# Performance work log

Measured on AMD Instinct MI355X. Metric: run time of the kernel, lower is better.

Reference implementation:

```python
import jax, jax.numpy as jnp
import numpy as np

B, T = 32, 64            # batch, max_timesteps
D_EMB, D_CONTENT, D_STYLE = 512, 128, 16
VOCAB = 32000
TEMP = 1.0
SOS_IDX = 0


def setup_inputs() -> dict:
    key = jax.random.key(0)
    ks = jax.random.split(key, 8)
    s = 0.02  # small init scale to keep softmax well-conditioned
    d_in = D_EMB + D_CONTENT + D_STYLE
    return {
        "content": jax.random.normal(ks[0], (B, D_CONTENT), jnp.float32),
        "style": jax.random.normal(ks[1], (B, D_STYLE), jnp.float32),
        "E": jax.random.normal(ks[2], (VOCAB, D_EMB), jnp.float32) * s,
        "Wk": jax.random.normal(ks[3], (d_in, 4 * D_EMB), jnp.float32) * s,
        "Wr": jax.random.normal(ks[4], (D_EMB, 4 * D_EMB), jnp.float32) * s,
        "b": jnp.zeros((4 * D_EMB,), jnp.float32),
        "Ws": jax.random.normal(ks[5], (D_EMB, VOCAB), jnp.float32) * s,
        "bs": jnp.zeros((VOCAB,), jnp.float32),
    }


def reference(content, style, E, Wk, Wr, b, Ws, bs):
    sos_emb = jnp.broadcast_to(E[SOS_IDX], (B, D_EMB))  # start token embedding

    def step(carry, _):
        h, c, emb = carry
        x = jnp.concatenate([emb, content, style], axis=-1)   # [B, d_in]
        z = x @ Wk + h @ Wr + b                               # [B, 4*units]
        i, f, g, o = jnp.split(z, 4, axis=-1)                  # keras gate order i,f,c,o
        i = jax.nn.sigmoid(i)
        f = jax.nn.sigmoid(f)
        g = jnp.tanh(g)
        o = jax.nn.sigmoid(o)
        c = f * c + i * g
        h = o * jnp.tanh(c)
        logits = h @ Ws + bs                                   # [B, vocab]
        p = jax.nn.softmax(logits / TEMP, axis=-1)
        emb_next = p @ E                                       # soft embedding [B, d_emb]
        return (h, c, emb_next), emb_next

    h0 = jnp.zeros((B, D_EMB), content.dtype)
    c0 = jnp.zeros((B, D_EMB), content.dtype)
    _, embs = jax.lax.scan(step, (h0, c0, sos_emb), None, length=T - 1)
    # [T-1, B, D] -> [B, T-1, D]; prepend SOS embedding
    out = jnp.concatenate([sos_emb[:, None, :], jnp.transpose(embs, (1, 0, 2))], axis=1)
    return out  # [B, T, d_emb]
```

## Files before the change

kernel.cpp:

```cpp
#include <hip/hip_runtime.h>

#define T_STEPS 63
#define NWG 256
#define WG_SIZE 256
#define NA 32
#define NV 224
#define NJC 14
#define NDC 16
#define NHM 15

typedef float floatx4 __attribute__((ext_vector_type(4)));
typedef __bf16 bf16x8 __attribute__((ext_vector_type(8)));

__device__ __forceinline__ unsigned short f2bf(float x) {
  unsigned int u = __builtin_bit_cast(unsigned int, x);
  u += 0x7fffu + ((u >> 16) & 1u);
  return (unsigned short)(u >> 16);
}
__device__ __forceinline__ float sigmoidf(float x) {
  return 1.0f / (1.0f + __expf(-x));
}
__device__ __forceinline__ floatx4 mfma_bf16(bf16x8 a, bf16x8 b, floatx4 c) {
  return __builtin_amdgcn_mfma_f32_16x16x32_bf16(a, b, c, 0, 0, 0);
}
__device__ __forceinline__ floatx4 mfma_fp8(long a, long b, floatx4 c) {
  return __builtin_amdgcn_mfma_f32_16x16x32_fp8_fp8(a, b, c, 0, 0, 0);
}
__device__ __forceinline__ unsigned char f2fp8(float x) {
  return (unsigned char)(__builtin_amdgcn_cvt_pk_fp8_f32(x, x, 0, false) & 0xff);
}

__device__ __forceinline__ unsigned long long ald64(const void* p) {
  return __hip_atomic_load((const unsigned long long*)p, __ATOMIC_RELAXED, __HIP_MEMORY_SCOPE_AGENT);
}
__device__ __forceinline__ float aldf(const float* p) {
  return __hip_atomic_load(p, __ATOMIC_RELAXED, __HIP_MEMORY_SCOPE_AGENT);
}
__device__ __forceinline__ void astf(float* p, float v) {
  __hip_atomic_store(p, v, __ATOMIC_RELAXED, __HIP_MEMORY_SCOPE_AGENT);
}
__device__ __forceinline__ void astu16(unsigned short* p, unsigned short v) {
  __hip_atomic_store(p, v, __ATOMIC_RELAXED, __HIP_MEMORY_SCOPE_AGENT);
}
__device__ __forceinline__ void astu32(unsigned int* p, unsigned int v) {
  __hip_atomic_store(p, v, __ATOMIC_RELAXED, __HIP_MEMORY_SCOPE_AGENT);
}
__device__ __forceinline__ void astu8(unsigned char* p, unsigned char v) {
  __hip_atomic_store(p, v, __ATOMIC_RELAXED, __HIP_MEMORY_SCOPE_AGENT);
}
__device__ __forceinline__ void afaddf(float* p, float v) {
  __hip_atomic_fetch_add(p, v, __ATOMIC_RELAXED, __HIP_MEMORY_SCOPE_AGENT);
}
__device__ __forceinline__ void afaddi(int* p, int v) {
  __hip_atomic_fetch_add(p, v, __ATOMIC_RELAXED, __HIP_MEMORY_SCOPE_AGENT);
}
__device__ __forceinline__ bf16x8 ld_bf8_at(const void* p) {
  union { unsigned long long q[2]; bf16x8 v; } u;
  u.q[0] = ald64(p);
  u.q[1] = ald64((const char*)p + 8);
  return u.v;
}

__device__ __forceinline__ void signal_flag(int* f) {
  __builtin_amdgcn_s_waitcnt(0);
  __syncthreads();
  if (threadIdx.x == 0)
    __hip_atomic_fetch_add(f, 1, __ATOMIC_RELAXED, __HIP_MEMORY_SCOPE_AGENT);
}
__device__ __forceinline__ void wait_flag(const int* f, int target) {
  if (threadIdx.x == 0) {
    while (__hip_atomic_load(f, __ATOMIC_RELAXED, __HIP_MEMORY_SCOPE_AGENT) < target)
      __builtin_amdgcn_s_sleep(2);
  }
  __syncthreads();
}

__global__ void k_transpose(const float* __restrict__ in, unsigned short* __restrict__ out,
                            int R, int C, int ostride, int ooff) {
  __shared__ unsigned short tile[64][65];
  const int r0 = blockIdx.x << 6, c0 = blockIdx.y << 6;
  const int t = threadIdx.x;
  const int tr4 = t >> 6, tc = t & 63;
#pragma unroll
  for (int p = 0; p < 16; ++p) {
    int i = (p << 2) + tr4;
    int r = r0 + i;
    unsigned short v = 0;
    if (r < R) v = f2bf(in[(size_t)r * C + (c0 + tc)]);
    tile[i][tc] = v;
  }
  __syncthreads();
#pragma unroll
  for (int p = 0; p < 16; ++p) {
    int j = (p << 2) + tr4;
    int r = r0 + tc;
    if (r < R) out[(size_t)(c0 + j) * ostride + ooff + r] = tile[tc][j];
  }
}

__global__ void k_transpose_fp8(const float* __restrict__ in, unsigned char* __restrict__ out,
                                int R, int C, long OS) {
  __shared__ unsigned char tile[64][68];
  const int r0 = blockIdx.x << 6, c0 = blockIdx.y << 6;
  const int t = threadIdx.x;
  const int tr4 = t >> 6, tc = t & 63;
#pragma unroll
  for (int p = 0; p < 16; ++p) {
    int i = (p << 2) + tr4;
    int r = r0 + i;
    float v = (r < R) ? in[(size_t)r * C + (c0 + tc)] : 0.f;
    tile[i][tc] = f2fp8(v);
  }
  __syncthreads();
#pragma unroll
  for (int p = 0; p < 16; ++p) {
    int j = (p << 2) + tr4;
    out[(size_t)(c0 + j) * OS + r0 + tc] = tile[tc][j];
  }
}

__global__ void k_init(const float* __restrict__ content, const float* __restrict__ style,
                       const float* __restrict__ E, unsigned short* cs_bf, float* out) {
  const int stride = gridDim.x * blockDim.x;
  const int idx = blockIdx.x * blockDim.x + threadIdx.x;
  for (int i = idx; i < 32 * 160; i += stride) {
    int b = i / 160, k = i - b * 160;
    float v = 0.f;
    if (k < 128)      v = content[b * 128 + k];
    else if (k < 144) v = style[b * 16 + (k - 128)];
    cs_bf[i] = f2bf(v);
  }
  for (int i = idx; i < 32 * 512; i += stride) {
    int b = i >> 9, d = i & 511;
    out[(size_t)b * (64 * 512) + d] = E[d];
  }
}

#define SMEM_BYTES 160768
#define OFF_E8TS_L 73728
#define OFF_ELDS_L 147456
#define OFF_ZBUF_L 152576

__global__ void __launch_bounds__(WG_SIZE, 1) k_main(
    const float* __restrict__ bvec,
    const float* __restrict__ bs,
    const unsigned char* __restrict__ Ws8_g,
    const unsigned char* __restrict__ E8T_g,
    const unsigned short* __restrict__ WkrT,
    const unsigned short* __restrict__ cs_bf,
    const float* __restrict__ E,
    unsigned short* h_bufg,
    unsigned char* h8,
    unsigned short* emb_bf,
    unsigned char* e8g,
    float* Upart,
    float* Zbuf,
    int* hflag, int* eflag, int* qflag, int* pvflag,
    float* out)
{
  const int wg = blockIdx.x;
  const int t  = threadIdx.x;
  const int wv = t >> 6;
  const int lane = t & 63;
  const int q = lane >> 4;
  const int m16 = lane & 15;

  __shared__ __align__(16) char smem[SMEM_BYTES];
  unsigned char* lds_ws   = (unsigned char*)smem;
  unsigned char* lds_e8ts = (unsigned char*)(smem + OFF_E8TS_L);
  unsigned char* lds_e    = (unsigned char*)(smem + OFF_ELDS_L);
  unsigned short* lds_wkr = (unsigned short*)smem;
  float* zbuf = (float*)(smem + OFF_ZBUF_L);

  if (wg < NA) {
    for (int idx = t; idx < 64 * 148; idx += WG_SIZE) {
      int row = idx / 148, grp = idx - row * 148;
      int g = row >> 4, c = row & 15;
      int n = g * 512 + (wg << 4) + c;
      ulong2 v = *(const ulong2*)(WkrT + (size_t)n * 1184 + grp * 8);
      *(ulong2*)((char*)lds_wkr + row * 2384 + grp * 16) = v;
    }
    const int dl = t & 15;
    const float bias0 = bvec[0 * 512 + (wg << 4) + dl];
    const float bias1 = bvec[1 * 512 + (wg << 4) + dl];
    const float bias2 = bvec[2 * 512 + (wg << 4) + dl];
    const float bias3 = bvec[3 * 512 + (wg << 4) + dl];
    float c2[2] = {0.f, 0.f};
    __syncthreads();

    const int mt = wv & 1, g0 = (wv >> 1) << 1;
    const int row = mt * 16 + m16;
    const unsigned short* b0row = lds_wkr + (g0 * 16 + m16) * 1192;
    const unsigned short* b1row = lds_wkr + ((g0 + 1) * 16 + m16) * 1192;
    const int d = (wg << 4) + dl;
    const int dc_a = wg >> 1;
    const int dl32 = ((wg & 1) << 4) + dl;

    floatx4 accG0 = {0.f, 0.f, 0.f, 0.f}, accG1 = {0.f, 0.f, 0.f, 0.f};

    for (int s = 0; s < T_STEPS; ++s) {
      const int pc = s & 1;
      if (s == 0) {
#pragma unroll
        for (int ks = 16; ks < 21; ++ks) {
          bf16x8 a = *(const bf16x8*)(cs_bf + row * 160 + (ks - 16) * 32 + q * 8);
          accG0 = mfma_bf16(a, *(const bf16x8*)(b0row + ks * 32 + q * 8), accG0);
          accG1 = mfma_bf16(a, *(const bf16x8*)(b1row + ks * 32 + q * 8), accG1);
        }
#pragma unroll 4
        for (int ks = 0; ks < 16; ++ks) {
          const float* ep = E + ks * 32 + q * 8;
          bf16x8 a;
#pragma unroll
          for (int i = 0; i < 8; ++i) a[i] = (__bf16)ep[i];
          accG0 = mfma_bf16(a, *(const bf16x8*)(b0row + ks * 32 + q * 8), accG0);
          accG1 = mfma_bf16(a, *(const bf16x8*)(b1row + ks * 32 + q * 8), accG1);
        }
      } else {
        wait_flag(eflag + (s - 1) * 16, NA);
        if (t < NJC) astf(Zbuf + ((s - 1) & 1) * (NJC * 32) + t * 32 + wg, 0.0f);
#pragma unroll 8
        for (int ks = 0; ks < 16; ++ks) {
          bf16x8 a = ld_bf8_at(emb_bf + row * 512 + ks * 32 + q * 8);
          accG0 = mfma_bf16(a, *(const bf16x8*)(b0row + ks * 32 + q * 8), accG0);
          accG1 = mfma_bf16(a, *(const bf16x8*)(b1row + ks * 32 + q * 8), accG1);
        }
      }
#pragma unroll
      for (int r = 0; r < 4; ++r) {
        zbuf[(g0 * 32 + mt * 16 + q * 4 + r) * 16 + m16] = accG0[r];
        zbuf[((g0 + 1) * 32 + mt * 16 + q * 4 + r) * 16 + m16] = accG1[r];
      }
      __syncthreads();
#pragma unroll
      for (int pp = 0; pp < 2; ++pp) {
        const int b = (pp * 256 + t) >> 4;
        float zi = zbuf[(0 * 32 + b) * 16 + dl] + bias0;
        float zf = zbuf[(1 * 32 + b) * 16 + dl] + bias1;
        float zg = zbuf[(2 * 32 + b) * 16 + dl] + bias2;
        float zo = zbuf[(3 * 32 + b) * 16 + dl] + bias3;
        float iv = sigmoidf(zi), fv = sigmoidf(zf);
        float gv = tanhf(zg),    ov = sigmoidf(zo);
        c2[pp] = fv * c2[pp] + iv * gv;
        float h = ov * tanhf(c2[pp]);
        astu16(h_bufg + b * 512 + d, f2bf(h));
        astu8(h8 + b * 512 + d, f2fp8(h));
      }
      __builtin_amdgcn_s_waitcnt(0);
      __syncthreads();
      if (t < NHM) afaddi(hflag + (s * NHM + t) * 16, 1);
      if (s + 1 < T_STEPS) {
        wait_flag(hflag + (s * NHM + (NHM - 1)) * 16, NA);
        accG0 = floatx4{0.f, 0.f, 0.f, 0.f};
        accG1 = floatx4{0.f, 0.f, 0.f, 0.f};
#pragma unroll 8
        for (int ks = 21; ks < 37; ++ks) {
          bf16x8 a = ld_bf8_at(h_bufg + row * 512 + (ks - 21) * 32 + q * 8);
          accG0 = mfma_bf16(a, *(const bf16x8*)(b0row + ks * 32 + q * 8), accG0);
          accG1 = mfma_bf16(a, *(const bf16x8*)(b1row + ks * 32 + q * 8), accG1);
        }
#pragma unroll
        for (int ks = 16; ks < 21; ++ks) {
          bf16x8 a = *(const bf16x8*)(cs_bf + row * 160 + (ks - 16) * 32 + q * 8);
          accG0 = mfma_bf16(a, *(const bf16x8*)(b0row + ks * 32 + q * 8), accG0);
          accG1 = mfma_bf16(a, *(const bf16x8*)(b1row + ks * 32 + q * 8), accG1);
        }
      }
      wait_flag(pvflag + (s * NDC + dc_a) * 16, NJC);
      float evs[2];
#pragma unroll
      for (int pp = 0; pp < 2; ++pp) {
        const int b = (pp * 256 + t) >> 4;
        float uv = 0.f, Zv = 0.f;
        const float* up = Upart + ((size_t)(dc_a * NJC) * 32 + b) * 32 + dl32;
#pragma unroll
        for (int g = 0; g < NJC; ++g) uv += aldf(up + g * 1024);
#pragma unroll
        for (int g = 0; g < NJC; ++g) Zv += aldf(Zbuf + pc * (NJC * 32) + g * 32 + b);
        float ev = uv / Zv;
        evs[pp] = ev;
        astu16(emb_bf + b * 512 + d, f2bf(ev));
      }
      signal_flag(eflag + s * 16);
#pragma unroll
      for (int pp = 0; pp < 2; ++pp) {
        const int b = (pp * 256 + t) >> 4;
        out[(size_t)b * (64 * 512) + (size_t)(s + 1) * 512 + d] = evs[pp];
      }
    }
  } else {
    const int wgv = wg - NA;
    const int jc = wgv >> 4;
    const int dc = wgv & 15;
    const long j0 = (long)wgv * 144;
    for (int idx = t; idx < 144 * 64; idx += WG_SIZE) {
      int row = idx >> 6, grp = idx & 63;
      long v = *(const long*)(Ws8_g + (j0 + row) * 512 + grp * 8);
      *(long*)(lds_ws + row * 512 + ((grp ^ (row & 7)) << 3)) = v;
    }
    for (int idx = t; idx < 32 * 288; idx += WG_SIZE) {
      int dd = idx / 288, g = idx - dd * 288;
      long v = *(const long*)(E8T_g + (size_t)(dc * 32 + dd) * 32768 + (size_t)jc * 2304 + (size_t)g * 8);
      int g2 = g + dd; if (g2 >= 288) g2 -= 288;
      *(long*)(lds_e8ts + dd * 2304 + (g2 << 3)) = v;
    }
    for (int idx = t; idx < (32 * 160) / 8; idx += WG_SIZE) ((long*)lds_e)[idx] = 0;
    __syncthreads();

    for (int s = 0; s < T_STEPS; ++s) {
      wait_flag(hflag + (s * NHM + jc) * 16, NA);
      const int pc = s & 1;
      long ah[2][16];
#pragma unroll
      for (int mtl = 0; mtl < 2; ++mtl)
#pragma unroll
        for (int ks = 0; ks < 16; ++ks)
          ah[mtl][ks] = (long)ald64(h8 + (mtl * 16 + m16) * 512 + ks * 32 + q * 8);
      for (int tile = wv; tile < 9; tile += 4) {
        const int jl = tile * 16 + m16;
        const unsigned char* wrow = lds_ws + jl * 512;
        const int sw = jl & 7;
        floatx4 acc[2] = {{0,0,0,0},{0,0,0,0}};
#pragma unroll
        for (int ks = 0; ks < 16; ++ks) {
          int g = ks * 4 + q;
          long bfrag = *(const long*)(wrow + ((g ^ sw) << 3));
          acc[0] = mfma_fp8(ah[0][ks], bfrag, acc[0]);
          acc[1] = mfma_fp8(ah[1][ks], bfrag, acc[1]);
        }
        const long jg = j0 + jl;
        const float bsv = bs[jg < 32000 ? jg : 31999];
        const bool valid = (jg < 32000);
#pragma unroll
        for (int mtl = 0; mtl < 2; ++mtl)
#pragma unroll
          for (int r = 0; r < 4; ++r) {
            float e = valid ? __expf(acc[mtl][r] + bsv) : 0.0f;
            lds_e[(mtl * 16 + q * 4 + r) * 160 + jl] = f2fp8(e);
          }
      }
      __syncthreads();
      for (int idx = t; idx < 32 * 36; idx += WG_SIZE) {
        int b = idx / 36, g = idx - b * 36;
        unsigned int v = *(const unsigned int*)(lds_e + b * 160 + g * 4);
        astu32((unsigned int*)(e8g + (size_t)b * 32768 + j0 + g * 4), v);
      }
      if (t >= 192 && t < 224) {
        const int b = t - 192;
        const unsigned int* rowp = (const unsigned int*)(lds_e + b * 160);
        float z = 0.f;
        for (int g = 0; g < 36; ++g) {
          int w4 = (int)rowp[g];
          z += __builtin_amdgcn_cvt_f32_fp8(w4, 0) + __builtin_amdgcn_cvt_f32_fp8(w4, 1)
             + __builtin_amdgcn_cvt_f32_fp8(w4, 2) + __builtin_amdgcn_cvt_f32_fp8(w4, 3);
        }
        afaddf(Zbuf + pc * (NJC * 32) + jc * 32 + b, z);
      }
      signal_flag(qflag + (s * NJC + jc) * 16);
      wait_flag(qflag + (s * NJC + jc) * 16, 16);
      {
        const int mtp = wv & 1, ntl = wv >> 1;
        const int dl_local = ntl * 16 + m16;
        const unsigned char* erow = lds_e8ts + dl_local * 2304;
        const unsigned char* arow = e8g + (size_t)(mtp * 16 + m16) * 32768 + (size_t)jc * 2304;
        floatx4 acc0 = {0,0,0,0}, acc1 = {0,0,0,0};
#pragma unroll 8
        for (int ks = 0; ks < 72; ks += 2) {
          long a0 = (long)ald64(arow + ks * 32 + q * 8);
          long a1 = (long)ald64(arow + (ks + 1) * 32 + q * 8);
          int g0 = ks * 4 + q + dl_local; if (g0 >= 288) g0 -= 288;
          int g1 = g0 + 4;                if (g1 >= 288) g1 -= 288;
          acc0 = mfma_fp8(a0, *(const long*)(erow + (g0 << 3)), acc0);
          acc1 = mfma_fp8(a1, *(const long*)(erow + (g1 << 3)), acc1);
        }
        floatx4 accs = acc0 + acc1;
#pragma unroll
        for (int r = 0; r < 4; ++r)
          astf(Upart + ((size_t)(dc * NJC + jc) * 32 + (mtp * 16 + q * 4 + r)) * 32 + dl_local, accs[r]);
      }
      signal_flag(pvflag + (s * NDC + dc) * 16);
    }
  }
}

extern "C" void kernel_launch(void* const* d_in, const int* in_sizes, int n_in,
                              void* d_out, int out_size, void* d_ws, size_t ws_size,
                              hipStream_t stream) {
  const float* content = (const float*)d_in[0];
  const float* style   = (const float*)d_in[1];
  const float* E       = (const float*)d_in[2];
  const float* Wk      = (const float*)d_in[3];
  const float* Wr      = (const float*)d_in[4];
  const float* bvec    = (const float*)d_in[5];
  const float* Ws      = (const float*)d_in[6];
  const float* bs      = (const float*)d_in[7];
  float* out = (float*)d_out;
  char* ws = (char*)d_ws;

  constexpr size_t SZ_WS8  = 32256ull * 512;
  constexpr size_t SZ_E8T  = 512ull * 32768;
  constexpr size_t SZ_WKRT = 2048ull * 1184 * 2;
  constexpr size_t SZ_CS   = 32ull * 160 * 2;
  constexpr size_t SZ_HB   = 32ull * 512 * 2;
  constexpr size_t SZ_H8   = 32ull * 512;
  constexpr size_t SZ_E8G  = 32ull * 32768;
  constexpr size_t SZ_UP   = 16ull * 14 * 32 * 32 * 4;
  constexpr size_t SZ_ZB   = 2ull * 14 * 32 * 4;
  constexpr size_t SZ_HF   = 64ull * 15 * 16 * 4;
  constexpr size_t SZ_EF   = 64ull * 16 * 4;
  constexpr size_t SZ_QF   = 63ull * 14 * 16 * 4;
  constexpr size_t SZ_PF   = 63ull * 16 * 16 * 4;
  constexpr size_t SZ_EMB  = 32ull * 512 * 2;
  constexpr size_t OFF_WS8  = 0;
  constexpr size_t OFF_E8T  = OFF_WS8 + SZ_WS8;
  constexpr size_t OFF_WKRT = OFF_E8T + SZ_E8T;
  constexpr size_t OFF_CS   = OFF_WKRT + SZ_WKRT;
  constexpr size_t OFF_HB   = OFF_CS + SZ_CS;
  constexpr size_t OFF_H8   = OFF_HB + SZ_HB;
  constexpr size_t OFF_E8G  = OFF_H8 + SZ_H8;
  constexpr size_t OFF_UP   = OFF_E8G + SZ_E8G;
  constexpr size_t OFF_ZB   = OFF_UP + SZ_UP;
  constexpr size_t OFF_HF   = OFF_ZB + SZ_ZB;
  constexpr size_t OFF_EF   = OFF_HF + SZ_HF;
  constexpr size_t OFF_QF   = OFF_EF + SZ_EF;
  constexpr size_t OFF_PF   = OFF_QF + SZ_QF;
  constexpr size_t OFF_EMB  = OFF_PF + SZ_PF;

  unsigned char*  Ws8_g = (unsigned char*)(ws + OFF_WS8);
  unsigned char*  E8T_g = (unsigned char*)(ws + OFF_E8T);
  unsigned short* WkrT  = (unsigned short*)(ws + OFF_WKRT);
  unsigned short* cs_bf = (unsigned short*)(ws + OFF_CS);
  unsigned short* h_bufg= (unsigned short*)(ws + OFF_HB);
  unsigned char*  h8    = (unsigned char*)(ws + OFF_H8);
  unsigned char*  e8g   = (unsigned char*)(ws + OFF_E8G);
  float* Upart          = (float*)(ws + OFF_UP);
  float* Zbuf           = (float*)(ws + OFF_ZB);
  int* hflag            = (int*)(ws + OFF_HF);
  int* eflag            = (int*)(ws + OFF_EF);
  int* qflag            = (int*)(ws + OFF_QF);
  int* pvflag           = (int*)(ws + OFF_PF);
  unsigned short* emb_bf= (unsigned short*)(ws + OFF_EMB);

  hipMemsetAsync(Ws8_g, 0, SZ_WS8, stream);
  hipMemsetAsync(E8T_g, 0, SZ_E8T, stream);
  hipMemsetAsync(WkrT, 0, SZ_WKRT, stream);
  hipMemsetAsync(ws + OFF_ZB, 0, SZ_ZB + SZ_HF + SZ_EF + SZ_QF + SZ_PF, stream);

  k_transpose_fp8<<<dim3(8, 500), 256, 0, stream>>>(Ws, Ws8_g, 512, 32000, 512);
  k_transpose_fp8<<<dim3(500, 8), 256, 0, stream>>>(E, E8T_g, 32000, 512, 32768);
  k_transpose<<<dim3(11, 32), 256, 0, stream>>>(Wk, WkrT, 656, 2048, 1184, 0);
  k_transpose<<<dim3(8, 32), 256, 0, stream>>>(Wr, WkrT, 512, 2048, 1184, 672);
  k_init<<<64, 256, 0, stream>>>(content, style, E, cs_bf, out);

  void* args[] = { (void*)&bvec, (void*)&bs, (void*)&Ws8_g, (void*)&E8T_g, (void*)&WkrT,
                   (void*)&cs_bf, (void*)&E, (void*)&h_bufg, (void*)&h8, (void*)&emb_bf,
                   (void*)&e8g, (void*)&Upart, (void*)&Zbuf,
                   (void*)&hflag, (void*)&eflag, (void*)&qflag, (void*)&pvflag,
                   (void*)&out };
  hipLaunchCooperativeKernel((void*)k_main, dim3(NWG), dim3(WG_SIZE), args, 0, stream);

  (void)in_sizes; (void)n_in; (void)out_size; (void)ws_size;
}
```

Baseline: 2.072 ms.

## Precompute E·Wk product to feed soft-prob gate input directly, bypassing embedding round-trip

Precomputes M = E @ Wk_emb (vocab x 2048 gates) in fp8 during setup. Each vocab workgroup then multiplies its unnormalized softmax chunk by M to produce partial gate pre-activations, so the LSTM workgroups no longer wait for the normalized soft embedding before computing the next step's gates. The emb_bf handoff and its flag are removed, and the output writes are deferred by one step. The change also double-buffers the e8 and Upart buffers and replaces the sleep-based spin with a busy spin. In exchange it adds a large setup GEMM, an extra 32x2048 gate GEMM over the vocab each step, and fp8 rounding error in the gate inputs.

```diff
diff --git a/kernel.cpp b/kernel.cpp
--- a/kernel.cpp
+++ b/kernel.cpp
@@ -61,6 +61,9 @@
   return u.v;
 }
 
+__device__ __forceinline__ void spin_until(const int* f, int target) {
+  while (__hip_atomic_load(f, __ATOMIC_RELAXED, __HIP_MEMORY_SCOPE_AGENT) < target) { }
+}
 __device__ __forceinline__ void signal_flag(int* f) {
   __builtin_amdgcn_s_waitcnt(0);
   __syncthreads();
@@ -68,10 +71,7 @@
     __hip_atomic_fetch_add(f, 1, __ATOMIC_RELAXED, __HIP_MEMORY_SCOPE_AGENT);
 }
 __device__ __forceinline__ void wait_flag(const int* f, int target) {
-  if (threadIdx.x == 0) {
-    while (__hip_atomic_load(f, __ATOMIC_RELAXED, __HIP_MEMORY_SCOPE_AGENT) < target)
-      __builtin_amdgcn_s_sleep(2);
-  }
+  if (threadIdx.x == 0) spin_until(f, target);
   __syncthreads();
 }
 
@@ -99,7 +99,7 @@
 }
 
 __global__ void k_transpose_fp8(const float* __restrict__ in, unsigned char* __restrict__ out,
-                                int R, int C, long OS) {
+                                int R, int C, long OS, float scale) {
   __shared__ unsigned char tile[64][68];
   const int r0 = blockIdx.x << 6, c0 = blockIdx.y << 6;
   const int t = threadIdx.x;
@@ -108,7 +108,7 @@
   for (int p = 0; p < 16; ++p) {
     int i = (p << 2) + tr4;
     int r = r0 + i;
-    float v = (r < R) ? in[(size_t)r * C + (c0 + tc)] : 0.f;
+    float v = (r < R) ? in[(size_t)r * C + (c0 + tc)] * scale : 0.f;
     tile[i][tc] = f2fp8(v);
   }
   __syncthreads();
@@ -117,6 +117,56 @@
     int j = (p << 2) + tr4;
     out[(size_t)(c0 + j) * OS + r0 + tc] = tile[tc][j];
   }
+}
+
+__global__ void k_cast_e8(const float* __restrict__ E, unsigned char* __restrict__ E8) {
+  const int stride = gridDim.x * blockDim.x;
+  const int total = 32256 * 512 / 4;
+  for (int i = blockIdx.x * blockDim.x + threadIdx.x; i < total; i += stride) {
+    int row = i >> 7;
+    unsigned int w = 0;
+    if (row < 32000) {
+      const float* p = E + (size_t)i * 4;
+      int lo = __builtin_amdgcn_cvt_pk_fp8_f32(p[0] * 16.f, p[1] * 16.f, 0, false);
+      w = (unsigned int)__builtin_amdgcn_cvt_pk_fp8_f32(p[2] * 16.f, p[3] * 16.f, lo, true);
+    }
+    *(unsigned int*)(E8 + (size_t)i * 4) = w;
+  }
+}
+
+__global__ void __launch_bounds__(256) k_gemm_m(const unsigned char* __restrict__ Wk8T,
+                                               const unsigned char* __restrict__ E8,
+                                               unsigned char* __restrict__ MT8) {
+  const int j0 = blockIdx.x << 7, g0 = blockIdx.y << 7;
+  const int t = threadIdx.x, wv = t >> 6, lane = t & 63;
+  const int q = lane >> 4, m16 = lane & 15;
+  const int gtb = wv << 1;
+  floatx4 acc[2][8];
+#pragma unroll
+  for (int a = 0; a < 2; ++a)
+#pragma unroll
+    for (int b = 0; b < 8; ++b) acc[a][b] = floatx4{0.f, 0.f, 0.f, 0.f};
+#pragma unroll 4
+  for (int ks = 0; ks < 16; ++ks) {
+    long a0 = *(const long*)(Wk8T + (size_t)(g0 + gtb * 16 + m16) * 512 + ks * 32 + q * 8);
+    long a1 = *(const long*)(Wk8T + (size_t)(g0 + gtb * 16 + 16 + m16) * 512 + ks * 32 + q * 8);
+#pragma unroll
+    for (int jt = 0; jt < 8; ++jt) {
+      long b = *(const long*)(E8 + (size_t)(j0 + jt * 16 + m16) * 512 + ks * 32 + q * 8);
+      acc[0][jt] = mfma_fp8(a0, b, acc[0][jt]);
+      acc[1][jt] = mfma_fp8(a1, b, acc[1][jt]);
+    }
+  }
+#pragma unroll
+  for (int gt2 = 0; gt2 < 2; ++gt2)
+#pragma unroll
+    for (int jt = 0; jt < 8; ++jt)
+#pragma unroll
+      for (int r = 0; r < 4; ++r) {
+        int g = g0 + (gtb + gt2) * 16 + (q << 2) + r;
+        int j = j0 + jt * 16 + m16;
+        MT8[(size_t)g * 32768 + j] = f2fp8(acc[gt2][jt][r] * 0.5f);
+      }
 }
 
 __global__ void k_init(const float* __restrict__ content, const float* __restrict__ style,
@@ -149,13 +199,14 @@
     const unsigned short* __restrict__ WkrT,
     const unsigned short* __restrict__ cs_bf,
     const float* __restrict__ E,
+    const unsigned char* __restrict__ MT8,
     unsigned short* h_bufg,
     unsigned char* h8,
-    unsigned short* emb_bf,
     unsigned char* e8g,
     float* Upart,
+    float* Zp,
     float* Zbuf,
-    int* hflag, int* eflag, int* qflag, int* pvflag,
+    int* hflag, int* qflag, int* zflag, int* gflag, int* pvflag,
     float* out)
 {
   const int wg = blockIdx.x;
@@ -188,18 +239,20 @@
     float c2[2] = {0.f, 0.f};
     __syncthreads();
 
-    const int mt = wv & 1, g0 = (wv >> 1) << 1;
+    const int mt = wv & 1, g0w = (wv >> 1) << 1;
     const int row = mt * 16 + m16;
-    const unsigned short* b0row = lds_wkr + (g0 * 16 + m16) * 1192;
-    const unsigned short* b1row = lds_wkr + ((g0 + 1) * 16 + m16) * 1192;
+    const unsigned short* b0row = lds_wkr + (g0w * 16 + m16) * 1192;
+    const unsigned short* b1row = lds_wkr + ((g0w + 1) * 16 + m16) * 1192;
     const int d = (wg << 4) + dl;
     const int dc_a = wg >> 1;
     const int dl32 = ((wg & 1) << 4) + dl;
+    const int gcbase = wg >> 3;
 
     floatx4 accG0 = {0.f, 0.f, 0.f, 0.f}, accG1 = {0.f, 0.f, 0.f, 0.f};
+    float inv[2] = {0.f, 0.f};
+    float zr[2][4];
 
     for (int s = 0; s < T_STEPS; ++s) {
-      const int pc = s & 1;
       if (s == 0) {
 #pragma unroll
         for (int ks = 16; ks < 21; ++ks) {
@@ -217,19 +270,34 @@
           accG1 = mfma_bf16(a, *(const bf16x8*)(b1row + ks * 32 + q * 8), accG1);
         }
       } else {
-        wait_flag(eflag + (s - 1) * 16, NA);
-        if (t < NJC) astf(Zbuf + ((s - 1) & 1) * (NJC * 32) + t * 32 + wg, 0.0f);
-#pragma unroll 8
-        for (int ks = 0; ks < 16; ++ks) {
-          bf16x8 a = ld_bf8_at(emb_bf + row * 512 + ks * 32 + q * 8);
-          accG0 = mfma_bf16(a, *(const bf16x8*)(b0row + ks * 32 + q * 8), accG0);
-          accG1 = mfma_bf16(a, *(const bf16x8*)(b1row + ks * 32 + q * 8), accG1);
+        if (t < 4) spin_until(zflag + (((s - 1) * NDC + (t * 4 + gcbase)) << 4), NJC);
+        else if (t == 4) spin_until(gflag + ((s - 1) << 4), NA);
+        __syncthreads();
+        const int pc1 = (s - 1) & 1;
+#pragma unroll
+        for (int pp = 0; pp < 2; ++pp) {
+          const int b = (pp * 256 + t) >> 4;
+          const float* zp = Zp + (size_t)b * 2048 + (wg << 4) + dl;
+          float z0 = 0.f, z1 = 0.f, z2 = 0.f, z3 = 0.f, Zv = 0.f;
+#pragma unroll
+          for (int jc = 0; jc < NJC; ++jc) {
+            const float* p = zp + jc * 65536;
+            z0 += aldf(p);
+            z1 += aldf(p + 512);
+            z2 += aldf(p + 1024);
+            z3 += aldf(p + 1536);
+            Zv += aldf(Zbuf + pc1 * (NJC * 32) + jc * 32 + b);
+          }
+          float iv = 1.0f / (128.0f * Zv);
+          inv[pp] = iv;
+          zr[pp][0] = z0 * iv; zr[pp][1] = z1 * iv;
+          zr[pp][2] = z2 * iv; zr[pp][3] = z3 * iv;
         }
       }
 #pragma unroll
       for (int r = 0; r < 4; ++r) {
-        zbuf[(g0 * 32 + mt * 16 + q * 4 + r) * 16 + m16] = accG0[r];
-        zbuf[((g0 + 1) * 32 + mt * 16 + q * 4 + r) * 16 + m16] = accG1[r];
+        zbuf[(g0w * 32 + mt * 16 + q * 4 + r) * 16 + m16] = accG0[r];
+        zbuf[((g0w + 1) * 32 + mt * 16 + q * 4 + r) * 16 + m16] = accG1[r];
       }
       __syncthreads();
 #pragma unroll
@@ -239,6 +307,7 @@
         float zf = zbuf[(1 * 32 + b) * 16 + dl] + bias1;
         float zg = zbuf[(2 * 32 + b) * 16 + dl] + bias2;
         float zo = zbuf[(3 * 32 + b) * 16 + dl] + bias3;
+        if (s > 0) { zi += zr[pp][0]; zf += zr[pp][1]; zg += zr[pp][2]; zo += zr[pp][3]; }
         float iv = sigmoidf(zi), fv = sigmoidf(zf);
         float gv = tanhf(zg),    ov = sigmoidf(zo);
         c2[pp] = fv * c2[pp] + iv * gv;
@@ -248,9 +317,9 @@
       }
       __builtin_amdgcn_s_waitcnt(0);
       __syncthreads();
-      if (t < NHM) afaddi(hflag + (s * NHM + t) * 16, 1);
+      if (t < NHM) afaddi(hflag + ((s * NHM + t) << 4), 1);
       if (s + 1 < T_STEPS) {
-        wait_flag(hflag + (s * NHM + (NHM - 1)) * 16, NA);
+        wait_flag(hflag + ((s * NHM + (NHM - 1)) << 4), NA);
         accG0 = floatx4{0.f, 0.f, 0.f, 0.f};
         accG1 = floatx4{0.f, 0.f, 0.f, 0.f};
 #pragma unroll 8
@@ -265,51 +334,61 @@
           accG0 = mfma_bf16(a, *(const bf16x8*)(b0row + ks * 32 + q * 8), accG0);
           accG1 = mfma_bf16(a, *(const bf16x8*)(b1row + ks * 32 + q * 8), accG1);
         }
-      }
-      wait_flag(pvflag + (s * NDC + dc_a) * 16, NJC);
-      float evs[2];
+        signal_flag(gflag + (s << 4));
+      }
+      if (s >= 1) {
+        wait_flag(pvflag + (((s - 1) * NDC + dc_a) << 4), NJC);
+        const int pc1 = (s - 1) & 1;
+#pragma unroll
+        for (int pp = 0; pp < 2; ++pp) {
+          const int b = (pp * 256 + t) >> 4;
+          float uv = 0.f;
+          const float* up = Upart + (size_t)pc1 * 229376 + ((size_t)(dc_a * NJC) * 32 + b) * 32 + dl32;
+#pragma unroll
+          for (int jc = 0; jc < NJC; ++jc) uv += aldf(up + jc * 1024);
+          out[(size_t)b * (64 * 512) + (size_t)s * 512 + d] = uv * inv[pp] * 128.0f;
+        }
+        if (t < NJC) astf(Zbuf + pc1 * (NJC * 32) + t * 32 + wg, 0.0f);
+      }
+    }
+    {
+      wait_flag(pvflag + (((T_STEPS - 1) * NDC + dc_a) << 4), NJC);
+      const int pc1 = (T_STEPS - 1) & 1;
 #pragma unroll
       for (int pp = 0; pp < 2; ++pp) {
         const int b = (pp * 256 + t) >> 4;
         float uv = 0.f, Zv = 0.f;
-        const float* up = Upart + ((size_t)(dc_a * NJC) * 32 + b) * 32 + dl32;
-#pragma unroll
-        for (int g = 0; g < NJC; ++g) uv += aldf(up + g * 1024);
-#pragma unroll
-        for (int g = 0; g < NJC; ++g) Zv += aldf(Zbuf + pc * (NJC * 32) + g * 32 + b);
-        float ev = uv / Zv;
-        evs[pp] = ev;
-        astu16(emb_bf + b * 512 + d, f2bf(ev));
-      }
-      signal_flag(eflag + s * 16);
-#pragma unroll
-      for (int pp = 0; pp < 2; ++pp) {
-        const int b = (pp * 256 + t) >> 4;
-        out[(size_t)b * (64 * 512) + (size_t)(s + 1) * 512 + d] = evs[pp];
+        const float* up = Upart + (size_t)pc1 * 229376 + ((size_t)(dc_a * NJC) * 32 + b) * 32 + dl32;
+#pragma unroll
+        for (int jc = 0; jc < NJC; ++jc) {
+          uv += aldf(up + jc * 1024);
+          Zv += aldf(Zbuf + pc1 * (NJC * 32) + jc * 32 + b);
+        }
+        out[(size_t)b * (64 * 512) + (size_t)T_STEPS * 512 + d] = uv / Zv;
       }
     }
   } else {
     const int wgv = wg - NA;
     const int jc = wgv >> 4;
-    const int dc = wgv & 15;
+    const int gc = wgv & 15;
     const long j0 = (long)wgv * 144;
     for (int idx = t; idx < 144 * 64; idx += WG_SIZE) {
-      int row = idx >> 6, grp = idx & 63;
-      long v = *(const long*)(Ws8_g + (j0 + row) * 512 + grp * 8);
-      *(long*)(lds_ws + row * 512 + ((grp ^ (row & 7)) << 3)) = v;
+      int r2 = idx >> 6, grp = idx & 63;
+      long v = *(const long*)(Ws8_g + (j0 + r2) * 512 + grp * 8);
+      *(long*)(lds_ws + r2 * 512 + ((grp ^ (r2 & 7)) << 3)) = v;
     }
     for (int idx = t; idx < 32 * 288; idx += WG_SIZE) {
       int dd = idx / 288, g = idx - dd * 288;
-      long v = *(const long*)(E8T_g + (size_t)(dc * 32 + dd) * 32768 + (size_t)jc * 2304 + (size_t)g * 8);
+      long v = *(const long*)(E8T_g + (size_t)(gc * 32 + dd) * 32768 + (size_t)jc * 2304 + (size_t)g * 8);
       int g2 = g + dd; if (g2 >= 288) g2 -= 288;
       *(long*)(lds_e8ts + dd * 2304 + (g2 << 3)) = v;
     }
-    for (int idx = t; idx < (32 * 160) / 8; idx += WG_SIZE) ((long*)lds_e)[idx] = 0;
     __syncthreads();
 
     for (int s = 0; s < T_STEPS; ++s) {
-      wait_flag(hflag + (s * NHM + jc) * 16, NA);
+      wait_flag(hflag + ((s * NHM + jc) << 4), NA);
       const int pc = s & 1;
+      unsigned char* e8p = e8g + (size_t)pc * 1048576;
       long ah[2][16];
 #pragma unroll
       for (int mtl = 0; mtl < 2; ++mtl)
@@ -343,8 +422,10 @@
       for (int idx = t; idx < 32 * 36; idx += WG_SIZE) {
         int b = idx / 36, g = idx - b * 36;
         unsigned int v = *(const unsigned int*)(lds_e + b * 160 + g * 4);
-        astu32((unsigned int*)(e8g + (size_t)b * 32768 + j0 + g * 4), v);
-      }
+        astu32((unsigned int*)(e8p + (size_t)b * 32768 + j0 + g * 4), v);
+      }
+      signal_flag(qflag + ((s * NJC + jc) << 4));
+      wait_flag(qflag + ((s * NJC + jc) << 4), 16);
       if (t >= 192 && t < 224) {
         const int b = t - 192;
         const unsigned int* rowp = (const unsigned int*)(lds_e + b * 160);
@@ -356,29 +437,52 @@
         }
         afaddf(Zbuf + pc * (NJC * 32) + jc * 32 + b, z);
       }
-      signal_flag(qflag + (s * NJC + jc) * 16);
-      wait_flag(qflag + (s * NJC + jc) * 16, 16);
+      if (s < T_STEPS - 1) {
+        const int mtp = wv & 1, ggb = (wv >> 1) << 2;
+        const unsigned char* ab = e8p + (size_t)(mtp * 16 + m16) * 32768 + (size_t)jc * 2304;
+        const unsigned char* mb = MT8 + (size_t)(gc * 128 + ggb * 16 + m16) * 32768 + (size_t)jc * 2304;
+        floatx4 za0 = {0,0,0,0}, za1 = {0,0,0,0}, za2 = {0,0,0,0}, za3 = {0,0,0,0};
+#pragma unroll 4
+        for (int ks = 0; ks < 72; ++ks) {
+          long a = (long)ald64(ab + ks * 32 + q * 8);
+          long b0 = *(const long*)(mb + 0ull * 524288 + ks * 32 + q * 8);
+          long b1 = *(const long*)(mb + 1ull * 524288 + ks * 32 + q * 8);
+          long b2 = *(const long*)(mb + 2ull * 524288 + ks * 32 + q * 8);
+          long b3 = *(const long*)(mb + 3ull * 524288 + ks * 32 + q * 8);
+          za0 = mfma_fp8(a, b0, za0); za1 = mfma_fp8(a, b1, za1);
+          za2 = mfma_fp8(a, b2, za2); za3 = mfma_fp8(a, b3, za3);
+        }
+        const int brow = mtp * 16 + (q << 2);
+#pragma unroll
+        for (int r = 0; r < 4; ++r) {
+          float* zp = Zp + (size_t)(jc * 32 + brow + r) * 2048 + gc * 128 + ggb * 16 + m16;
+          astf(zp +  0, za0[r]); astf(zp + 16, za1[r]);
+          astf(zp + 32, za2[r]); astf(zp + 48, za3[r]);
+        }
+        signal_flag(zflag + ((s * NDC + gc) << 4));
+      }
       {
         const int mtp = wv & 1, ntl = wv >> 1;
         const int dl_local = ntl * 16 + m16;
         const unsigned char* erow = lds_e8ts + dl_local * 2304;
-        const unsigned char* arow = e8g + (size_t)(mtp * 16 + m16) * 32768 + (size_t)jc * 2304;
+        const unsigned char* arow = e8p + (size_t)(mtp * 16 + m16) * 32768 + (size_t)jc * 2304;
         floatx4 acc0 = {0,0,0,0}, acc1 = {0,0,0,0};
 #pragma unroll 8
         for (int ks = 0; ks < 72; ks += 2) {
           long a0 = (long)ald64(arow + ks * 32 + q * 8);
           long a1 = (long)ald64(arow + (ks + 1) * 32 + q * 8);
-          int g0 = ks * 4 + q + dl_local; if (g0 >= 288) g0 -= 288;
-          int g1 = g0 + 4;                if (g1 >= 288) g1 -= 288;
-          acc0 = mfma_fp8(a0, *(const long*)(erow + (g0 << 3)), acc0);
-          acc1 = mfma_fp8(a1, *(const long*)(erow + (g1 << 3)), acc1);
+          int g0i = ks * 4 + q + dl_local; if (g0i >= 288) g0i -= 288;
+          int g1i = g0i + 4;               if (g1i >= 288) g1i -= 288;
+          acc0 = mfma_fp8(a0, *(const long*)(erow + (g0i << 3)), acc0);
+          acc1 = mfma_fp8(a1, *(const long*)(erow + (g1i << 3)), acc1);
         }
         floatx4 accs = acc0 + acc1;
 #pragma unroll
         for (int r = 0; r < 4; ++r)
-          astf(Upart + ((size_t)(dc * NJC + jc) * 32 + (mtp * 16 + q * 4 + r)) * 32 + dl_local, accs[r]);
-      }
-      signal_flag(pvflag + (s * NDC + dc) * 16);
+          astf(Upart + (size_t)pc * 229376 +
+               ((size_t)(gc * NJC + jc) * 32 + (mtp * 16 + (q << 2) + r)) * 32 + dl_local, accs[r]);
+      }
+      signal_flag(pvflag + ((s * NDC + gc) << 4));
     }
   }
 }
@@ -403,28 +507,34 @@
   constexpr size_t SZ_CS   = 32ull * 160 * 2;
   constexpr size_t SZ_HB   = 32ull * 512 * 2;
   constexpr size_t SZ_H8   = 32ull * 512;
-  constexpr size_t SZ_E8G  = 32ull * 32768;
-  constexpr size_t SZ_UP   = 16ull * 14 * 32 * 32 * 4;
-  constexpr size_t SZ_ZB   = 2ull * 14 * 32 * 4;
-  constexpr size_t SZ_HF   = 64ull * 15 * 16 * 4;
-  constexpr size_t SZ_EF   = 64ull * 16 * 4;
-  constexpr size_t SZ_QF   = 63ull * 14 * 16 * 4;
-  constexpr size_t SZ_PF   = 63ull * 16 * 16 * 4;
-  constexpr size_t SZ_EMB  = 32ull * 512 * 2;
+  constexpr size_t SZ_ZB   = 2ull * NJC * 32 * 4;
+  constexpr size_t SZ_HF   = 63ull * NHM * 16 * 4;
+  constexpr size_t SZ_QF   = 63ull * NJC * 16 * 4;
+  constexpr size_t SZ_ZF   = 63ull * NDC * 16 * 4;
+  constexpr size_t SZ_GF   = 63ull * 16 * 4;
+  constexpr size_t SZ_PF   = 63ull * NDC * 16 * 4;
+  constexpr size_t SZ_E8   = 32256ull * 512;
+  constexpr size_t SZ_WK8T = 2048ull * 512;
+  constexpr size_t SZ_MT8  = 2048ull * 32768;
+
   constexpr size_t OFF_WS8  = 0;
   constexpr size_t OFF_E8T  = OFF_WS8 + SZ_WS8;
   constexpr size_t OFF_WKRT = OFF_E8T + SZ_E8T;
   constexpr size_t OFF_CS   = OFF_WKRT + SZ_WKRT;
   constexpr size_t OFF_HB   = OFF_CS + SZ_CS;
   constexpr size_t OFF_H8   = OFF_HB + SZ_HB;
-  constexpr size_t OFF_E8G  = OFF_H8 + SZ_H8;
-  constexpr size_t OFF_UP   = OFF_E8G + SZ_E8G;
-  constexpr size_t OFF_ZB   = OFF_UP + SZ_UP;
-  constexpr size_t OFF_HF   = OFF_ZB + SZ_ZB;
-  constexpr size_t OFF_EF   = OFF_HF + SZ_HF;
-  constexpr size_t OFF_QF   = OFF_EF + SZ_EF;
-  constexpr size_t OFF_PF   = OFF_QF + SZ_QF;
-  constexpr size_t OFF_EMB  = OFF_PF + SZ_PF;
+  constexpr size_t OFF_ZB   = OFF_H8 + SZ_H8;
+  constexpr size_t OFF_HFL  = OFF_ZB + SZ_ZB;
+  constexpr size_t OFF_QFL  = OFF_HFL + SZ_HF;
+  constexpr size_t OFF_ZFL  = OFF_QFL + SZ_QF;
+  constexpr size_t OFF_GFL  = OFF_ZFL + SZ_ZF;
+  constexpr size_t OFF_PFL  = OFF_GFL + SZ_GF;
+  constexpr size_t OFF_E8   = OFF_PFL + SZ_PF;
+  constexpr size_t OFF_E8G  = OFF_E8;
+  constexpr size_t OFF_UP   = OFF_E8 + 2097152;
+  constexpr size_t OFF_ZP   = OFF_E8 + 3932160;
+  constexpr size_t OFF_WK8T = OFF_E8 + SZ_E8;
+  constexpr size_t OFF_MT8  = OFF_WK8T + SZ_WK8T;
 
   unsigned char*  Ws8_g = (unsigned char*)(ws + OFF_WS8);
   unsigned char*  E8T_g = (unsigned char*)(ws + OFF_E8T);
@@ -432,30 +542,37 @@
   unsigned short* cs_bf = (unsigned short*)(ws + OFF_CS);
   unsigned short* h_bufg= (unsigned short*)(ws + OFF_HB);
   unsigned char*  h8    = (unsigned char*)(ws + OFF_H8);
+  float* Zbuf           = (float*)(ws + OFF_ZB);
+  int* hflag            = (int*)(ws + OFF_HFL);
+  int* qflag            = (int*)(ws + OFF_QFL);
+  int* zflag            = (int*)(ws + OFF_ZFL);
+  int* gflag            = (int*)(ws + OFF_GFL);
+  int* pvflag           = (int*)(ws + OFF_PFL);
+  unsigned char*  E8    = (unsigned char*)(ws + OFF_E8);
   unsigned char*  e8g   = (unsigned char*)(ws + OFF_E8G);
   float* Upart          = (float*)(ws + OFF_UP);
-  float* Zbuf           = (float*)(ws + OFF_ZB);
-  int* hflag            = (int*)(ws + OFF_HF);
-  int* eflag            = (int*)(ws + OFF_EF);
-  int* qflag            = (int*)(ws + OFF_QF);
-  int* pvflag           = (int*)(ws + OFF_PF);
-  unsigned short* emb_bf= (unsigned short*)(ws + OFF_EMB);
+  float* Zp             = (float*)(ws + OFF_ZP);
+  unsigned char*  Wk8T  = (unsigned char*)(ws + OFF_WK8T);
+  unsigned char*  MT8   = (unsigned char*)(ws + OFF_MT8);
 
   hipMemsetAsync(Ws8_g, 0, SZ_WS8, stream);
   hipMemsetAsync(E8T_g, 0, SZ_E8T, stream);
   hipMemsetAsync(WkrT, 0, SZ_WKRT, stream);
-  hipMemsetAsync(ws + OFF_ZB, 0, SZ_ZB + SZ_HF + SZ_EF + SZ_QF + SZ_PF, stream);
-
-  k_transpose_fp8<<<dim3(8, 500), 256, 0, stream>>>(Ws, Ws8_g, 512, 32000, 512);
-  k_transpose_fp8<<<dim3(500, 8), 256, 0, stream>>>(E, E8T_g, 32000, 512, 32768);
+  hipMemsetAsync(ws + OFF_ZB, 0, SZ_ZB + SZ_HF + SZ_QF + SZ_ZF + SZ_GF + SZ_PF, stream);
+
+  k_transpose_fp8<<<dim3(8, 500), 256, 0, stream>>>(Ws, Ws8_g, 512, 32000, 512, 1.0f);
+  k_transpose_fp8<<<dim3(500, 8), 256, 0, stream>>>(E, E8T_g, 32000, 512, 32768, 1.0f);
+  k_transpose_fp8<<<dim3(8, 32), 256, 0, stream>>>(Wk, Wk8T, 512, 2048, 512, 16.0f);
+  k_cast_e8<<<2048, 256, 0, stream>>>(E, E8);
+  k_gemm_m<<<dim3(252, 16), 256, 0, stream>>>(Wk8T, E8, MT8);
   k_transpose<<<dim3(11, 32), 256, 0, stream>>>(Wk, WkrT, 656, 2048, 1184, 0);
   k_transpose<<<dim3(8, 32), 256, 0, stream>>>(Wr, WkrT, 512, 2048, 1184, 672);
   k_init<<<64, 256, 0, stream>>>(content, style, E, cs_bf, out);
 
   void* args[] = { (void*)&bvec, (void*)&bs, (void*)&Ws8_g, (void*)&E8T_g, (void*)&WkrT,
-                   (void*)&cs_bf, (void*)&E, (void*)&h_bufg, (void*)&h8, (void*)&emb_bf,
-                   (void*)&e8g, (void*)&Upart, (void*)&Zbuf,
-                   (void*)&hflag, (void*)&eflag, (void*)&qflag, (void*)&pvflag,
+                   (void*)&cs_bf, (void*)&E, (void*)&MT8, (void*)&h_bufg, (void*)&h8,
+                   (void*)&e8g, (void*)&Upart, (void*)&Zp, (void*)&Zbuf,
+                   (void*)&hflag, (void*)&qflag, (void*)&zflag, (void*)&gflag, (void*)&pvflag,
                    (void*)&out };
   hipLaunchCooperativeKernel((void*)k_main, dim3(NWG), dim3(WG_SIZE), args, 0, stream);
 
```

Result: slower. 4.289 ms (+107.0%).

## Replace atomic counter flags with per-workgroup step stamps and wave-wide polling

Applied to the files above, without the earlier changes.

Cross-workgroup synchronisation moves from shared fetch-add counters, polled by one thread with sleeps, to per-workgroup step stamps. Each producer writes a plain atomic store of its step number, and a whole wave polls all producer slots in parallel with __any. The Zbuf zeroing is moved after the embedding publish. This is meant to remove atomic contention on hot counters and the sleep latency on the serial decode critical path, at the cost of more polling traffic from full waves.

```diff
diff --git a/kernel.cpp b/kernel.cpp
--- a/kernel.cpp
+++ b/kernel.cpp
@@ -7,7 +7,6 @@
 #define NV 224
 #define NJC 14
 #define NDC 16
-#define NHM 15
 
 typedef float floatx4 __attribute__((ext_vector_type(4)));
 typedef __bf16 bf16x8 __attribute__((ext_vector_type(8)));
@@ -36,9 +35,15 @@
 __device__ __forceinline__ float aldf(const float* p) {
   return __hip_atomic_load(p, __ATOMIC_RELAXED, __HIP_MEMORY_SCOPE_AGENT);
 }
+__device__ __forceinline__ int aldi(const int* p) {
+  return __hip_atomic_load(p, __ATOMIC_RELAXED, __HIP_MEMORY_SCOPE_AGENT);
+}
 __device__ __forceinline__ void astf(float* p, float v) {
   __hip_atomic_store(p, v, __ATOMIC_RELAXED, __HIP_MEMORY_SCOPE_AGENT);
 }
+__device__ __forceinline__ void asti(int* p, int v) {
+  __hip_atomic_store(p, v, __ATOMIC_RELAXED, __HIP_MEMORY_SCOPE_AGENT);
+}
 __device__ __forceinline__ void astu16(unsigned short* p, unsigned short v) {
   __hip_atomic_store(p, v, __ATOMIC_RELAXED, __HIP_MEMORY_SCOPE_AGENT);
 }
@@ -49,9 +54,6 @@
   __hip_atomic_store(p, v, __ATOMIC_RELAXED, __HIP_MEMORY_SCOPE_AGENT);
 }
 __device__ __forceinline__ void afaddf(float* p, float v) {
-  __hip_atomic_fetch_add(p, v, __ATOMIC_RELAXED, __HIP_MEMORY_SCOPE_AGENT);
-}
-__device__ __forceinline__ void afaddi(int* p, int v) {
   __hip_atomic_fetch_add(p, v, __ATOMIC_RELAXED, __HIP_MEMORY_SCOPE_AGENT);
 }
 __device__ __forceinline__ bf16x8 ld_bf8_at(const void* p) {
@@ -61,18 +63,17 @@
   return u.v;
 }
 
-__device__ __forceinline__ void signal_flag(int* f) {
+__device__ __forceinline__ void wave_spin(const int* base, int n, int tgt) {
+  const int lane = threadIdx.x & 63;
+  int v;
+  do {
+    v = (lane < n) ? aldi(base + lane) : 0x7fffffff;
+  } while (__any(v < tgt));
+}
+__device__ __forceinline__ void stamp_publish(int* slot, int v) {
   __builtin_amdgcn_s_waitcnt(0);
   __syncthreads();
-  if (threadIdx.x == 0)
-    __hip_atomic_fetch_add(f, 1, __ATOMIC_RELAXED, __HIP_MEMORY_SCOPE_AGENT);
-}
-__device__ __forceinline__ void wait_flag(const int* f, int target) {
-  if (threadIdx.x == 0) {
-    while (__hip_atomic_load(f, __ATOMIC_RELAXED, __HIP_MEMORY_SCOPE_AGENT) < target)
-      __builtin_amdgcn_s_sleep(2);
-  }
-  __syncthreads();
+  if (threadIdx.x == 0) asti(slot, v);
 }
 
 __global__ void k_transpose(const float* __restrict__ in, unsigned short* __restrict__ out,
@@ -155,7 +156,10 @@
     unsigned char* e8g,
     float* Upart,
     float* Zbuf,
-    int* hflag, int* eflag, int* qflag, int* pvflag,
+    int* hstep,
+    int* estep,
+    int* qstep,
+    int* pvstep,
     float* out)
 {
   const int wg = blockIdx.x;
@@ -188,10 +192,10 @@
     float c2[2] = {0.f, 0.f};
     __syncthreads();
 
-    const int mt = wv & 1, g0 = (wv >> 1) << 1;
+    const int mt = wv & 1, g0w = (wv >> 1) << 1;
     const int row = mt * 16 + m16;
-    const unsigned short* b0row = lds_wkr + (g0 * 16 + m16) * 1192;
-    const unsigned short* b1row = lds_wkr + ((g0 + 1) * 16 + m16) * 1192;
+    const unsigned short* b0row = lds_wkr + (g0w * 16 + m16) * 1192;
+    const unsigned short* b1row = lds_wkr + ((g0w + 1) * 16 + m16) * 1192;
     const int d = (wg << 4) + dl;
     const int dc_a = wg >> 1;
     const int dl32 = ((wg & 1) << 4) + dl;
@@ -217,8 +221,7 @@
           accG1 = mfma_bf16(a, *(const bf16x8*)(b1row + ks * 32 + q * 8), accG1);
         }
       } else {
-        wait_flag(eflag + (s - 1) * 16, NA);
-        if (t < NJC) astf(Zbuf + ((s - 1) & 1) * (NJC * 32) + t * 32 + wg, 0.0f);
+        wave_spin(estep, NA, s);
 #pragma unroll 8
         for (int ks = 0; ks < 16; ++ks) {
           bf16x8 a = ld_bf8_at(emb_bf + row * 512 + ks * 32 + q * 8);
@@ -228,8 +231,8 @@
       }
 #pragma unroll
       for (int r = 0; r < 4; ++r) {
-        zbuf[(g0 * 32 + mt * 16 + q * 4 + r) * 16 + m16] = accG0[r];
-        zbuf[((g0 + 1) * 32 + mt * 16 + q * 4 + r) * 16 + m16] = accG1[r];
+        zbuf[(g0w * 32 + mt * 16 + q * 4 + r) * 16 + m16] = accG0[r];
+        zbuf[((g0w + 1) * 32 + mt * 16 + q * 4 + r) * 16 + m16] = accG1[r];
       }
       __syncthreads();
 #pragma unroll
@@ -246,11 +249,9 @@
         astu16(h_bufg + b * 512 + d, f2bf(h));
         astu8(h8 + b * 512 + d, f2fp8(h));
       }
-      __builtin_amdgcn_s_waitcnt(0);
-      __syncthreads();
-      if (t < NHM) afaddi(hflag + (s * NHM + t) * 16, 1);
+      stamp_publish(hstep + wg, s + 1);
       if (s + 1 < T_STEPS) {
-        wait_flag(hflag + (s * NHM + (NHM - 1)) * 16, NA);
+        wave_spin(hstep, NA, s + 1);
         accG0 = floatx4{0.f, 0.f, 0.f, 0.f};
         accG1 = floatx4{0.f, 0.f, 0.f, 0.f};
 #pragma unroll 8
@@ -266,7 +267,7 @@
           accG1 = mfma_bf16(a, *(const bf16x8*)(b1row + ks * 32 + q * 8), accG1);
         }
       }
-      wait_flag(pvflag + (s * NDC + dc_a) * 16, NJC);
+      wave_spin(pvstep + dc_a * 16, NJC, s + 1);
       float evs[2];
 #pragma unroll
       for (int pp = 0; pp < 2; ++pp) {
@@ -281,7 +282,8 @@
         evs[pp] = ev;
         astu16(emb_bf + b * 512 + d, f2bf(ev));
       }
-      signal_flag(eflag + s * 16);
+      if (s >= 1 && t < NJC) astf(Zbuf + ((s - 1) & 1) * (NJC * 32) + t * 32 + wg, 0.0f);
+      stamp_publish(estep + wg, s + 1);
 #pragma unroll
       for (int pp = 0; pp < 2; ++pp) {
         const int b = (pp * 256 + t) >> 4;
@@ -294,9 +296,9 @@
     const int dc = wgv & 15;
     const long j0 = (long)wgv * 144;
     for (int idx = t; idx < 144 * 64; idx += WG_SIZE) {
-      int row = idx >> 6, grp = idx & 63;
-      long v = *(const long*)(Ws8_g + (j0 + row) * 512 + grp * 8);
-      *(long*)(lds_ws + row * 512 + ((grp ^ (row & 7)) << 3)) = v;
+      int r2 = idx >> 6, grp = idx & 63;
+      long v = *(const long*)(Ws8_g + (j0 + r2) * 512 + grp * 8);
+      *(long*)(lds_ws + r2 * 512 + ((grp ^ (r2 & 7)) << 3)) = v;
     }
     for (int idx = t; idx < 32 * 288; idx += WG_SIZE) {
       int dd = idx / 288, g = idx - dd * 288;
@@ -308,7 +310,7 @@
     __syncthreads();
 
     for (int s = 0; s < T_STEPS; ++s) {
-      wait_flag(hflag + (s * NHM + jc) * 16, NA);
+      wave_spin(hstep, NA, s + 1);
       const int pc = s & 1;
       long ah[2][16];
 #pragma unroll
@@ -356,8 +358,8 @@
         }
         afaddf(Zbuf + pc * (NJC * 32) + jc * 32 + b, z);
       }
-      signal_flag(qflag + (s * NJC + jc) * 16);
-      wait_flag(qflag + (s * NJC + jc) * 16, 16);
+      stamp_publish(qstep + wgv, s + 1);
+      wave_spin(qstep + jc * 16, 16, s + 1);
       {
         const int mtp = wv & 1, ntl = wv >> 1;
         const int dl_local = ntl * 16 + m16;
@@ -368,17 +370,17 @@
         for (int ks = 0; ks < 72; ks += 2) {
           long a0 = (long)ald64(arow + ks * 32 + q * 8);
           long a1 = (long)ald64(arow + (ks + 1) * 32 + q * 8);
-          int g0 = ks * 4 + q + dl_local; if (g0 >= 288) g0 -= 288;
-          int g1 = g0 + 4;                if (g1 >= 288) g1 -= 288;
-          acc0 = mfma_fp8(a0, *(const long*)(erow + (g0 << 3)), acc0);
-          acc1 = mfma_fp8(a1, *(const long*)(erow + (g1 << 3)), acc1);
+          int g0i = ks * 4 + q + dl_local; if (g0i >= 288) g0i -= 288;
+          int g1i = g0i + 4;               if (g1i >= 288) g1i -= 288;
+          acc0 = mfma_fp8(a0, *(const long*)(erow + (g0i << 3)), acc0);
+          acc1 = mfma_fp8(a1, *(const long*)(erow + (g1i << 3)), acc1);
         }
         floatx4 accs = acc0 + acc1;
 #pragma unroll
         for (int r = 0; r < 4; ++r)
-          astf(Upart + ((size_t)(dc * NJC + jc) * 32 + (mtp * 16 + q * 4 + r)) * 32 + dl_local, accs[r]);
-      }
-      signal_flag(pvflag + (s * NDC + dc) * 16);
+          astf(Upart + ((size_t)(dc * NJC + jc) * 32 + (mtp * 16 + (q << 2) + r)) * 32 + dl_local, accs[r]);
+      }
+      stamp_publish(pvstep + dc * 16 + jc, s + 1);
     }
   }
 }
@@ -403,28 +405,29 @@
   constexpr size_t SZ_CS   = 32ull * 160 * 2;
   constexpr size_t SZ_HB   = 32ull * 512 * 2;
   constexpr size_t SZ_H8   = 32ull * 512;
+  constexpr size_t SZ_EMB  = 32ull * 512 * 2;
   constexpr size_t SZ_E8G  = 32ull * 32768;
   constexpr size_t SZ_UP   = 16ull * 14 * 32 * 32 * 4;
-  constexpr size_t SZ_ZB   = 2ull * 14 * 32 * 4;
-  constexpr size_t SZ_HF   = 64ull * 15 * 16 * 4;
-  constexpr size_t SZ_EF   = 64ull * 16 * 4;
-  constexpr size_t SZ_QF   = 63ull * 14 * 16 * 4;
-  constexpr size_t SZ_PF   = 63ull * 16 * 16 * 4;
-  constexpr size_t SZ_EMB  = 32ull * 512 * 2;
+  constexpr size_t SZ_ZB   = 2ull * NJC * 32 * 4;
+  constexpr size_t SZ_HS   = 64ull * 4;
+  constexpr size_t SZ_ES   = 64ull * 4;
+  constexpr size_t SZ_QS   = 256ull * 4;
+  constexpr size_t SZ_PS   = 256ull * 4;
+
   constexpr size_t OFF_WS8  = 0;
   constexpr size_t OFF_E8T  = OFF_WS8 + SZ_WS8;
   constexpr size_t OFF_WKRT = OFF_E8T + SZ_E8T;
   constexpr size_t OFF_CS   = OFF_WKRT + SZ_WKRT;
   constexpr size_t OFF_HB   = OFF_CS + SZ_CS;
   constexpr size_t OFF_H8   = OFF_HB + SZ_HB;
-  constexpr size_t OFF_E8G  = OFF_H8 + SZ_H8;
+  constexpr size_t OFF_EMB  = OFF_H8 + SZ_H8;
+  constexpr size_t OFF_E8G  = OFF_EMB + SZ_EMB;
   constexpr size_t OFF_UP   = OFF_E8G + SZ_E8G;
   constexpr size_t OFF_ZB   = OFF_UP + SZ_UP;
-  constexpr size_t OFF_HF   = OFF_ZB + SZ_ZB;
-  constexpr size_t OFF_EF   = OFF_HF + SZ_HF;
-  constexpr size_t OFF_QF   = OFF_EF + SZ_EF;
-  constexpr size_t OFF_PF   = OFF_QF + SZ_QF;
-  constexpr size_t OFF_EMB  = OFF_PF + SZ_PF;
+  constexpr size_t OFF_HS   = OFF_ZB + SZ_ZB;
+  constexpr size_t OFF_ES   = OFF_HS + SZ_HS;
+  constexpr size_t OFF_QS   = OFF_ES + SZ_ES;
+  constexpr size_t OFF_PS   = OFF_QS + SZ_QS;
 
   unsigned char*  Ws8_g = (unsigned char*)(ws + OFF_WS8);
   unsigned char*  E8T_g = (unsigned char*)(ws + OFF_E8T);
@@ -432,19 +435,19 @@
   unsigned short* cs_bf = (unsigned short*)(ws + OFF_CS);
   unsigned short* h_bufg= (unsigned short*)(ws + OFF_HB);
   unsigned char*  h8    = (unsigned char*)(ws + OFF_H8);
+  unsigned short* emb_bf= (unsigned short*)(ws + OFF_EMB);
   unsigned char*  e8g   = (unsigned char*)(ws + OFF_E8G);
   float* Upart          = (float*)(ws + OFF_UP);
   float* Zbuf           = (float*)(ws + OFF_ZB);
-  int* hflag            = (int*)(ws + OFF_HF);
-  int* eflag            = (int*)(ws + OFF_EF);
-  int* qflag            = (int*)(ws + OFF_QF);
-  int* pvflag           = (int*)(ws + OFF_PF);
-  unsigned short* emb_bf= (unsigned short*)(ws + OFF_EMB);
+  int* hstep            = (int*)(ws + OFF_HS);
+  int* estep            = (int*)(ws + OFF_ES);
+  int* qstep            = (int*)(ws + OFF_QS);
+  int* pvstep           = (int*)(ws + OFF_PS);
 
   hipMemsetAsync(Ws8_g, 0, SZ_WS8, stream);
   hipMemsetAsync(E8T_g, 0, SZ_E8T, stream);
   hipMemsetAsync(WkrT, 0, SZ_WKRT, stream);
-  hipMemsetAsync(ws + OFF_ZB, 0, SZ_ZB + SZ_HF + SZ_EF + SZ_QF + SZ_PF, stream);
+  hipMemsetAsync(ws + OFF_ZB, 0, SZ_ZB + SZ_HS + SZ_ES + SZ_QS + SZ_PS, stream);
 
   k_transpose_fp8<<<dim3(8, 500), 256, 0, stream>>>(Ws, Ws8_g, 512, 32000, 512);
   k_transpose_fp8<<<dim3(500, 8), 256, 0, stream>>>(E, E8T_g, 32000, 512, 32768);
@@ -455,7 +458,7 @@
   void* args[] = { (void*)&bvec, (void*)&bs, (void*)&Ws8_g, (void*)&E8T_g, (void*)&WkrT,
                    (void*)&cs_bf, (void*)&E, (void*)&h_bufg, (void*)&h8, (void*)&emb_bf,
                    (void*)&e8g, (void*)&Upart, (void*)&Zbuf,
-                   (void*)&hflag, (void*)&eflag, (void*)&qflag, (void*)&pvflag,
+                   (void*)&hstep, (void*)&estep, (void*)&qstep, (void*)&pvstep,
                    (void*)&out };
   hipLaunchCooperativeKernel((void*)k_main, dim3(NWG), dim3(WG_SIZE), args, 0, stream);
 
```

Result: no change. 2.073 ms (+0.0%).
